# Kernel tuning notes

Hardware: AMD Instinct MI355X
Metric: run time of the kernel (lower is better)

Reference implementation:

```python
import jax, jax.numpy as jnp
import numpy as np

HIDDEN = 4544
NUM_HEADS = 71
HEAD_DIM = 64
SEQ = 2048
ROPE_BASE = 10000.0


def setup_inputs() -> dict:
    key = jax.random.key(0)
    k1, k2, k3 = jax.random.split(key, 3)
    hidden_states = jax.random.normal(k1, (1, 1, SEQ, HIDDEN), dtype=jnp.float32)
    # additive causal mask (0 on/below diagonal, -1e9 above)
    causal = jnp.tril(jnp.ones((SEQ, SEQ), dtype=bool))
    attention_mask = jnp.where(causal, 0.0, -1e9).astype(jnp.float32)[None, None]
    w_qkv = jax.random.normal(k2, (HIDDEN, (NUM_HEADS + 2) * HEAD_DIM), dtype=jnp.float32) * 0.02
    w_dense = jax.random.normal(k3, (HIDDEN, HIDDEN), dtype=jnp.float32) * 0.02
    # RoPE caches as in TtFalconRotaryEmbedding
    inv_freq = 1.0 / (ROPE_BASE ** (jnp.arange(0, HEAD_DIM, 2, dtype=jnp.float32) / HEAD_DIM))
    t = jnp.arange(SEQ, dtype=jnp.float32)
    freqs = jnp.outer(t, inv_freq)                      # [S, HD/2]
    emb = jnp.concatenate([freqs, freqs], axis=-1)      # [S, HD]
    return {
        "hidden_states": hidden_states,
        "attention_mask": attention_mask,
        "w_qkv": w_qkv,
        "w_dense": w_dense,
        "cos": jnp.cos(emb),
        "sin": jnp.sin(emb),
    }


def _rope(x, cos, sin):
    # x: [..., S, HD]; Falcon rotate_half: cat(-x2, x1)
    x1, x2 = jnp.split(x, 2, axis=-1)
    rot = jnp.concatenate([-x2, x1], axis=-1)
    return x * cos + rot * sin


def reference(hidden_states, attention_mask, w_qkv, w_dense, cos, sin):
    S = hidden_states.shape[2]
    x = hidden_states[0, 0]                              # [S, H]
    qkv = (x @ w_qkv).reshape(S, NUM_HEADS + 2, HEAD_DIM)
    q = jnp.transpose(qkv[:, :NUM_HEADS], (1, 0, 2))     # [nh, S, hd]
    k = qkv[:, NUM_HEADS]                                # [S, hd] (single MQA K head)
    v = qkv[:, NUM_HEADS + 1]                            # [S, hd]
    q = _rope(q, cos[None, :S], sin[None, :S])
    k = _rope(k, cos[:S], sin[:S])
    scale = 1.0 / np.sqrt(HEAD_DIM).astype(np.float32)
    scores = jnp.einsum('hsd,td->hst', q, k) * scale + attention_mask[0, 0][None]
    probs = jax.nn.softmax(scores, axis=-1)              # [nh, S, S]
    ctx = jnp.einsum('hst,td->hsd', probs, v)            # [nh, S, hd]
    out = jnp.transpose(ctx, (1, 0, 2)).reshape(S, NUM_HEADS * HEAD_DIM) @ w_dense
    return out[None, None]                               # [1, 1, S, H]
```

## Files before the change

kernel.cpp:

```cpp
#include <hip/hip_runtime.h>

typedef unsigned short u16;
typedef unsigned int u32;
typedef __attribute__((ext_vector_type(8))) __bf16 bf16x8;
typedef __attribute__((ext_vector_type(4))) float f32x4;

#define SEQ   2048
#define NH    71
#define HD    64
#define HID   4544
#define NQKV  4672
#define KP    4608
#define KSL   1536

__device__ __forceinline__ u16 f2bf(float f) {
    __bf16 b = (__bf16)f;
    return __builtin_bit_cast(u16, b);
}
__device__ __forceinline__ float bf2f(u16 u) {
    __bf16 b = __builtin_bit_cast(__bf16, u);
    return (float)b;
}

__device__ __forceinline__ void gload_lds16(const u16* g, u16* l) {
    __builtin_amdgcn_global_load_lds(
        (const __attribute__((address_space(1))) u32*)g,
        (__attribute__((address_space(3))) u32*)l, 16, 0, 0);
}

__global__ __launch_bounds__(256) void k_convert(const float* __restrict__ in,
                                                 u16* __restrict__ out) {
    const int row = blockIdx.x;
    const float* src = in + (size_t)row * HID;
    u16* dst = out + (size_t)row * KP;
    for (int c = threadIdx.x; c < KP / 8; c += 256) {
        u16 o[8];
        if (c < HID / 8) {
            float4 v0 = *(const float4*)(src + c * 8);
            float4 v1 = *(const float4*)(src + c * 8 + 4);
            o[0] = f2bf(v0.x); o[1] = f2bf(v0.y); o[2] = f2bf(v0.z); o[3] = f2bf(v0.w);
            o[4] = f2bf(v1.x); o[5] = f2bf(v1.y); o[6] = f2bf(v1.z); o[7] = f2bf(v1.w);
        } else {
#pragma unroll
            for (int j = 0; j < 8; ++j) o[j] = 0;
        }
        *(uint4*)(dst + c * 8) = *(uint4*)o;
    }
}

__global__ __launch_bounds__(256) void k_transpose(const float* __restrict__ in,
                                                   u16* __restrict__ out,
                                                   int R, int C, int Rp) {
    __shared__ float tile[32][33];
    int c0 = blockIdx.x * 32, r0 = blockIdx.y * 32;
    int tx = threadIdx.x & 31, ty = threadIdx.x >> 5;
#pragma unroll
    for (int i = 0; i < 32; i += 8) {
        int r = r0 + ty + i, c = c0 + tx;
        tile[ty + i][tx] = (r < R && c < C) ? in[(size_t)r * C + c] : 0.f;
    }
    __syncthreads();
#pragma unroll
    for (int i = 0; i < 32; i += 8)
        out[(size_t)(c0 + ty + i) * Rp + r0 + tx] = f2bf(tile[tx][ty + i]);
}

template <bool BF16OUT>
__global__ __launch_bounds__(512) void k_gemm_sk(const u16* __restrict__ A,
                                                 const u16* __restrict__ BT,
                                                 char* __restrict__ C0,
                                                 char* __restrict__ C1,
                                                 char* __restrict__ C2,
                                                 int N, int ntN) {
    __shared__ u16 ls[4][256 * 64];
    const int tid = threadIdx.x;
    const int lane = tid & 63;
    const int wid = tid >> 6;
    const int wr = wid >> 2, wc = wid & 3;
    const int l15 = lane & 15, lg = lane >> 4;

    const int p = blockIdx.x;
    const int m0 = (p & 7) * 256;
    const int rr_ = p >> 3;
    const int ks = rr_ / ntN;
    const int n0 = (rr_ % ntN) * 256;
    const int k0 = ks * KSL;

    const int sg = lane >> 3;
    const int slot = lane & 7;
    const u16* sb[4];
    int dstoff[4];
#pragma unroll
    for (int i = 0; i < 4; ++i) {
        int r = i * 64 + wid * 8 + sg;
        int sc = slot ^ (r & 7);
        sb[i] = (sc < 4) ? (A  + (size_t)(m0 + r) * KP + k0 + sc * 8)
                         : (BT + (size_t)(n0 + r) * KP + k0 + (sc ^ 4) * 8);
        dstoff[i] = r * 64 + slot * 8;
    }

    f32x4 acc[8][4];
#pragma unroll
    for (int i = 0; i < 8; ++i)
#pragma unroll
        for (int j = 0; j < 4; ++j) acc[i][j] = (f32x4){0.f, 0.f, 0.f, 0.f};

#define STG(d, kt, i) gload_lds16(sb[i] + (size_t)(kt) * 32, &ls[d][dstoff[i]])

    const int NT = KSL / 32;
    STG(0, 0, 0); STG(0, 0, 1); STG(0, 0, 2); STG(0, 0, 3);
    STG(1, 1, 0); STG(1, 1, 1); STG(1, 1, 2); STG(1, 1, 3);
    STG(2, 2, 0); STG(2, 2, 1); STG(2, 2, 2); STG(2, 2, 3);
    asm volatile("s_waitcnt vmcnt(8)" ::: "memory");
    __builtin_amdgcn_s_barrier();

    for (int kt = 0; kt < NT; ++kt) {
        const u16* L = ls[kt & 3];
        const int db = (kt + 3) & 3;
        const bool st = (kt + 3 < NT);
        bf16x8 bfr[4], af[4];
#pragma unroll
        for (int ni = 0; ni < 4; ++ni) {
            int rb = wc * 64 + ni * 16 + l15;
            bfr[ni] = *(const bf16x8*)(L + rb * 64 + ((lg ^ (rb & 7) ^ 4) << 3));
        }
#pragma unroll
        for (int mi = 0; mi < 4; ++mi) {
            int ra = wr * 128 + mi * 16 + l15;
            af[mi] = *(const bf16x8*)(L + ra * 64 + ((lg ^ (ra & 7)) << 3));
        }
        if (st) { STG(db, kt + 3, 0); STG(db, kt + 3, 1); }
        __builtin_amdgcn_s_barrier();
        __builtin_amdgcn_s_setprio(1);
#pragma unroll
        for (int mi = 0; mi < 4; ++mi)
#pragma unroll
            for (int ni = 0; ni < 4; ++ni)
                acc[mi][ni] = __builtin_amdgcn_mfma_f32_16x16x32_bf16(
                    af[mi], bfr[ni], acc[mi][ni], 0, 0, 0);
        __builtin_amdgcn_s_setprio(0);
        __builtin_amdgcn_s_barrier();
#pragma unroll
        for (int mi = 0; mi < 4; ++mi) {
            int ra = wr * 128 + (mi + 4) * 16 + l15;
            af[mi] = *(const bf16x8*)(L + ra * 64 + ((lg ^ (ra & 7)) << 3));
        }
        if (st) { STG(db, kt + 3, 2); STG(db, kt + 3, 3); }
        __builtin_amdgcn_s_barrier();
        __builtin_amdgcn_s_setprio(1);
#pragma unroll
        for (int mi = 0; mi < 4; ++mi)
#pragma unroll
            for (int ni = 0; ni < 4; ++ni)
                acc[mi + 4][ni] = __builtin_amdgcn_mfma_f32_16x16x32_bf16(
                    af[mi], bfr[ni], acc[mi + 4][ni], 0, 0, 0);
        __builtin_amdgcn_s_setprio(0);
        if (kt < NT - 3)       asm volatile("s_waitcnt vmcnt(8)" ::: "memory");
        else if (kt == NT - 3) asm volatile("s_waitcnt vmcnt(4)" ::: "memory");
        else if (kt == NT - 2) asm volatile("s_waitcnt vmcnt(0)" ::: "memory");
        __builtin_amdgcn_s_barrier();
    }
#undef STG

    char* Cks = (ks == 0) ? C0 : (ks == 1) ? C1 : C2;
#pragma unroll
    for (int mi = 0; mi < 8; ++mi)
#pragma unroll
        for (int ni = 0; ni < 4; ++ni) {
            int row = m0 + wr * 128 + mi * 16 + lg * 4;
            int col = n0 + wc * 64 + ni * 16 + l15;
            if (col < N) {
                if (BF16OUT) {
                    u16* Cb = (u16*)Cks;
#pragma unroll
                    for (int j = 0; j < 4; ++j)
                        Cb[(size_t)(row + j) * N + col] = f2bf(acc[mi][ni][j]);
                } else {
                    float* Cf = (float*)Cks;
#pragma unroll
                    for (int j = 0; j < 4; ++j)
                        Cf[(size_t)(row + j) * N + col] = acc[mi][ni][j];
                }
            }
        }
}

__global__ __launch_bounds__(256) void k_reduce(float* __restrict__ out,
                                                const float* __restrict__ P1,
                                                const float* __restrict__ P2, int n4) {
    for (int i = blockIdx.x * 256 + threadIdx.x; i < n4; i += gridDim.x * 256) {
        float4 a = ((const float4*)out)[i];
        float4 b = ((const float4*)P1)[i];
        float4 c = ((const float4*)P2)[i];
        a.x += b.x + c.x; a.y += b.y + c.y; a.z += b.z + c.z; a.w += b.w + c.w;
        ((float4*)out)[i] = a;
    }
}

__global__ __launch_bounds__(256) void k_rope(const u16* __restrict__ P0,
                                              const u16* __restrict__ P1,
                                              const u16* __restrict__ P2,
                                              const float* __restrict__ cosb,
                                              const float* __restrict__ sinb,
                                              u16* __restrict__ qb, u16* __restrict__ kb,
                                              u16* __restrict__ vT) {
    int s = blockIdx.x;
    __shared__ float row[NQKV];
    __shared__ float cs[64], sn[64];
    if (threadIdx.x < 64) {
        cs[threadIdx.x] = cosb[s * 64 + threadIdx.x];
        sn[threadIdx.x] = sinb[s * 64 + threadIdx.x];
    }
    const u16* r0 = P0 + (size_t)s * NQKV;
    const u16* r1 = P1 + (size_t)s * NQKV;
    const u16* r2 = P2 + (size_t)s * NQKV;
    for (int e = threadIdx.x; e < NQKV; e += 256)
        row[e] = bf2f(r0[e]) + bf2f(r1[e]) + bf2f(r2[e]);
    __syncthreads();
    const float qscale = 0.125f * 1.44269504f;
    for (int e = threadIdx.x; e < NQKV; e += 256) {
        int h = e >> 6, d = e & 63;
        float x = row[e];
        if (h < 72) {
            float other = row[h * 64 + ((d < 32) ? d + 32 : d - 32)];
            float rot = (d < 32) ? -other : other;
            float rr = x * cs[d] + rot * sn[d];
            if (h < NH) qb[((size_t)h * SEQ + s) * 64 + d] = f2bf(rr * qscale);
            else        kb[(size_t)s * 64 + d] = f2bf(rr);
        } else {
            vT[(size_t)d * SEQ + s] = f2bf(x);
        }
    }
}

__global__ __launch_bounds__(512) void k_attn(const u16* __restrict__ qb,
                                              const u16* __restrict__ kb,
                                              const u16* __restrict__ vT,
                                              u16* __restrict__ ctx) {
    const int tid = threadIdx.x;
    const int lane = tid & 63;
    const int wid = tid >> 6;
    const int l15 = lane & 15, lg = lane >> 4;

    const int bid = blockIdx.x;
    const int qt = 63 - bid / 9;
    const int hg = bid % 9;
    int h = hg * 8 + wid;
    const bool hval = (h < NH);
    if (!hval) h = NH - 1;
    const int q0 = qt * 32;
    const int nt = (qt >> 2) + 1;

    __shared__ u16 lsK[2][128 * 64];
    __shared__ u16 lsV[2][64 * 128];
    __shared__ u16 lsP[8][32 * 128];
    u16* myP = lsP[wid];

    const int kr = tid >> 3, kc = tid & 7;
    const int vd = tid >> 4, vc = tid & 15;

    bf16x8 qf[2][2];
#pragma unroll
    for (int mi = 0; mi < 2; ++mi)
#pragma unroll
        for (int ks = 0; ks < 2; ++ks)
            qf[mi][ks] = *(const bf16x8*)(qb + ((size_t)h * SEQ + q0 + mi * 16 + l15) * 64
                                          + ks * 32 + lg * 8);

    f32x4 oacc[2][4];
#pragma unroll
    for (int i = 0; i < 2; ++i)
#pragma unroll
        for (int j = 0; j < 4; ++j) oacc[i][j] = (f32x4){0.f, 0.f, 0.f, 0.f};
    float mrun[2] = {-3e38f, -3e38f};
    float lrun[2] = {0.f, 0.f};

    uint4 kg0, kg1, vg0, vg1;
    kg0 = *(const uint4*)(kb + (size_t)kr * 64 + kc * 8);
    kg1 = *(const uint4*)(kb + (size_t)(kr + 64) * 64 + kc * 8);
    vg0 = *(const uint4*)(vT + (size_t)vd * SEQ + vc * 8);
    vg1 = *(const uint4*)(vT + (size_t)(vd + 32) * SEQ + vc * 8);
    {
        const int kswz = (kr & 7) << 4;
        *(uint4*)((char*)lsK[0] + kr * 128 + ((kc * 16) ^ kswz)) = kg0;
        *(uint4*)((char*)lsK[0] + (kr + 64) * 128 + ((kc * 16) ^ kswz)) = kg1;
        *(uint4*)((char*)lsV[0] + vd * 256 + ((vc * 16) ^ ((vd & 15) << 4))) = vg0;
        *(uint4*)((char*)lsV[0] + (vd + 32) * 256 + ((vc * 16) ^ (((vd + 32) & 15) << 4))) = vg1;
    }

    for (int t = 0; t < nt; ++t) {
        const int t0 = t << 7;
        const int cb = t & 1;
        if (t + 1 < nt) {
            const int t1 = t0 + 128;
            kg0 = *(const uint4*)(kb + (size_t)(t1 + kr) * 64 + kc * 8);
            kg1 = *(const uint4*)(kb + (size_t)(t1 + kr + 64) * 64 + kc * 8);
            vg0 = *(const uint4*)(vT + (size_t)vd * SEQ + t1 + vc * 8);
            vg1 = *(const uint4*)(vT + (size_t)(vd + 32) * SEQ + t1 + vc * 8);
        }
        __syncthreads();

        f32x4 sacc[2][8];
#pragma unroll
        for (int i = 0; i < 2; ++i)
#pragma unroll
            for (int j = 0; j < 8; ++j) sacc[i][j] = (f32x4){0.f, 0.f, 0.f, 0.f};
#pragma unroll
        for (int ni = 0; ni < 8; ++ni) {
            const int rr = ni * 16 + l15;
            const int swz = (rr & 7) << 4;
            bf16x8 kf0 = *(const bf16x8*)((const char*)lsK[cb] + rr * 128 + ((lg * 16) ^ swz));
            bf16x8 kf1 = *(const bf16x8*)((const char*)lsK[cb] + rr * 128 + ((64 + lg * 16) ^ swz));
            sacc[0][ni] = __builtin_amdgcn_mfma_f32_16x16x32_bf16(kf0, qf[0][0], sacc[0][ni], 0, 0, 0);
            sacc[1][ni] = __builtin_amdgcn_mfma_f32_16x16x32_bf16(kf0, qf[1][0], sacc[1][ni], 0, 0, 0);
            sacc[0][ni] = __builtin_amdgcn_mfma_f32_16x16x32_bf16(kf1, qf[0][1], sacc[0][ni], 0, 0, 0);
            sacc[1][ni] = __builtin_amdgcn_mfma_f32_16x16x32_bf16(kf1, qf[1][1], sacc[1][ni], 0, 0, 0);
        }
        const bool last = (t == nt - 1);

#pragma unroll
        for (int mi = 0; mi < 2; ++mi) {
            const int q = q0 + mi * 16 + l15;
            if (last) {
#pragma unroll
                for (int ni = 0; ni < 8; ++ni)
#pragma unroll
                    for (int jj = 0; jj < 4; ++jj)
                        if (t0 + ni * 16 + lg * 4 + jj > q) sacc[mi][ni][jj] = -1e9f;
            }
            float m = sacc[mi][0][0];
#pragma unroll
            for (int ni = 0; ni < 8; ++ni)
#pragma unroll
                for (int jj = 0; jj < 4; ++jj) m = fmaxf(m, sacc[mi][ni][jj]);
            m = fmaxf(m, __shfl_xor(m, 16, 64));
            m = fmaxf(m, __shfl_xor(m, 32, 64));
            float mnew = fmaxf(mrun[mi], m);
            float alpha = exp2f(mrun[mi] - mnew);
            float rs = 0.f;
#pragma unroll
            for (int ni = 0; ni < 8; ++ni)
#pragma unroll
                for (int jj = 0; jj < 4; ++jj) {
                    float pp = exp2f(sacc[mi][ni][jj] - mnew);
                    sacc[mi][ni][jj] = pp;
                    rs += pp;
                }
            rs += __shfl_xor(rs, 16, 64);
            rs += __shfl_xor(rs, 32, 64);
            lrun[mi] = lrun[mi] * alpha + rs;
            mrun[mi] = mnew;

            const int qh = mi * 16 + l15;
            const int pswz = (qh & 7) << 4;
#pragma unroll
            for (int ni = 0; ni < 8; ++ni) {
                u32 w0 = (u32)f2bf(sacc[mi][ni][0]) | ((u32)f2bf(sacc[mi][ni][1]) << 16);
                u32 w1 = (u32)f2bf(sacc[mi][ni][2]) | ((u32)f2bf(sacc[mi][ni][3]) << 16);
                uint2 w; w.x = w0; w.y = w1;
                *(uint2*)((char*)myP + qh * 256 + ((ni * 32 + lg * 8) ^ pswz)) = w;
            }
#pragma unroll
            for (int jj = 0; jj < 4; ++jj) {
                float aB = __shfl(alpha, (lane & 48) + ((lane >> 4) & 3) * 4 + jj, 64);
#pragma unroll
                for (int nd = 0; nd < 4; ++nd) oacc[mi][nd][jj] *= aB;
            }
        }

#pragma unroll
        for (int ks = 0; ks < 4; ++ks) {
            bf16x8 pf[2];
#pragma unroll
            for (int mi = 0; mi < 2; ++mi) {
                const int qh = mi * 16 + l15;
                pf[mi] = *(const bf16x8*)((const char*)myP + qh * 256
                                          + ((ks * 64 + lg * 16) ^ ((qh & 7) << 4)));
            }
#pragma unroll
            for (int nd = 0; nd < 4; ++nd) {
                const int rr = nd * 16 + l15;
                bf16x8 vf = *(const bf16x8*)((const char*)lsV[cb] + rr * 256
                                             + ((ks * 64 + lg * 16) ^ ((rr & 15) << 4)));
                oacc[0][nd] = __builtin_amdgcn_mfma_f32_16x16x32_bf16(pf[0], vf, oacc[0][nd], 0, 0, 0);
                oacc[1][nd] = __builtin_amdgcn_mfma_f32_16x16x32_bf16(pf[1], vf, oacc[1][nd], 0, 0, 0);
            }
        }

        if (t + 1 < nt) {
            const int nb = cb ^ 1;
            const int kswz = (kr & 7) << 4;
            *(uint4*)((char*)lsK[nb] + kr * 128 + ((kc * 16) ^ kswz)) = kg0;
            *(uint4*)((char*)lsK[nb] + (kr + 64) * 128 + ((kc * 16) ^ kswz)) = kg1;
            *(uint4*)((char*)lsV[nb] + vd * 256 + ((vc * 16) ^ ((vd & 15) << 4))) = vg0;
            *(uint4*)((char*)lsV[nb] + (vd + 32) * 256 + ((vc * 16) ^ (((vd + 32) & 15) << 4))) = vg1;
        }
    }

    if (hval) {
#pragma unroll
        for (int mi = 0; mi < 2; ++mi)
#pragma unroll
            for (int jj = 0; jj < 4; ++jj) {
                float lB = __shfl(lrun[mi], (lane & 48) + ((lane >> 4) & 3) * 4 + jj, 64);
                float inv = 1.0f / lB;
                int q = q0 + mi * 16 + lg * 4 + jj;
#pragma unroll
                for (int nd = 0; nd < 4; ++nd)
                    ctx[(size_t)q * KP + h * 64 + nd * 16 + l15] = f2bf(oacc[mi][nd][jj] * inv);
            }
    } else {
#pragma unroll
        for (int mi = 0; mi < 2; ++mi)
#pragma unroll
            for (int jj = 0; jj < 4; ++jj) {
                int q = q0 + mi * 16 + lg * 4 + jj;
#pragma unroll
                for (int nd = 0; nd < 4; ++nd)
                    ctx[(size_t)q * KP + HID + nd * 16 + l15] = 0;
            }
    }
}

extern "C" void kernel_launch(void* const* d_in, const int* in_sizes, int n_in,
                              void* d_out, int out_size, void* d_ws, size_t ws_size,
                              hipStream_t stream) {
    const float* hs      = (const float*)d_in[0];
    const float* w_qkv   = (const float*)d_in[2];
    const float* w_dense = (const float*)d_in[3];
    const float* cosb    = (const float*)d_in[4];
    const float* sinb    = (const float*)d_in[5];
    float* out = (float*)d_out;

    char* ws = (char*)d_ws;
    u16*   x_bf  = (u16*)(ws + 0);
    u16*   wT    = (u16*)(ws + 18874368);
    char*  qP0   = ws + 63700992;
    char*  qP1   = ws + 82837504;
    char*  qP2   = ws + 101974016;
    u16*   q_bf  = (u16*)(ws + 121110528);
    u16*   k_bf  = (u16*)(ws + 139722752);
    u16*   vT_bf = (u16*)(ws + 139984896);
    char*  dP1   = ws + 63700992;
    char*  dP2   = ws + 100925440;

    k_convert<<<2048, 256, 0, stream>>>(hs, x_bf);
    k_transpose<<<dim3(152, 144), 256, 0, stream>>>(w_qkv, wT, HID, NQKV, KP);
    k_gemm_sk<true><<<dim3(456), 512, 0, stream>>>(x_bf, wT, qP0, qP1, qP2, NQKV, 19);
    k_rope<<<SEQ, 256, 0, stream>>>((const u16*)qP0, (const u16*)qP1, (const u16*)qP2,
                                    cosb, sinb, q_bf, k_bf, vT_bf);
    k_attn<<<dim3(576), 512, 0, stream>>>(q_bf, k_bf, vT_bf, x_bf );
    k_transpose<<<dim3(144, 144), 256, 0, stream>>>(w_dense, wT, HID, HID, KP);
    k_gemm_sk<false><<<dim3(432), 512, 0, stream>>>(x_bf , wT,
                                                    (char*)out, dP1, dP2, HID, 18);
    k_reduce<<<2048, 256, 0, stream>>>(out, (const float*)dP1, (const float*)dP2,
                                       SEQ * HID / 4);
}
```

Measured before the change: 417.1 us.

## Switch split-K GEMM to 32x32x16 MFMA and raise priority in attention MFMA loops

The GEMM inner loop now uses 32x32x16 bf16 MFMA tiles instead of 16x16x32. Each wave covers the same 128x64 output with fewer, larger instructions, and the K=32 step is split into two 16-wide halves with matching LDS fragment loads and a rewritten output indexing. The goal is fewer LDS fragment reads and higher MFMA throughput per instruction. Separately, the attention kernel wraps its QK and PV MFMA blocks in s_setprio so they get scheduling priority over other waves. The risk is higher accumulator register use and mistakes in the new fragment and output mapping.

```diff
diff --git a/kernel.cpp b/kernel.cpp
--- a/kernel.cpp
+++ b/kernel.cpp
@@ -4,6 +4,7 @@
 typedef unsigned int u32;
 typedef __attribute__((ext_vector_type(8))) __bf16 bf16x8;
 typedef __attribute__((ext_vector_type(4))) float f32x4;
+typedef __attribute__((ext_vector_type(16))) float f32x16;
 
 #define SEQ   2048
 #define NH    71
@@ -77,7 +78,7 @@
     const int lane = tid & 63;
     const int wid = tid >> 6;
     const int wr = wid >> 2, wc = wid & 3;
-    const int l15 = lane & 15, lg = lane >> 4;
+    const int l31 = lane & 31, hi = lane >> 5;
 
     const int p = blockIdx.x;
     const int m0 = (p & 7) * 256;
@@ -99,11 +100,11 @@
         dstoff[i] = r * 64 + slot * 8;
     }
 
-    f32x4 acc[8][4];
+    f32x16 acc[8];
 #pragma unroll
     for (int i = 0; i < 8; ++i)
 #pragma unroll
-        for (int j = 0; j < 4; ++j) acc[i][j] = (f32x4){0.f, 0.f, 0.f, 0.f};
+        for (int j = 0; j < 16; ++j) acc[i][j] = 0.f;
 
 #define STG(d, kt, i) gload_lds16(sb[i] + (size_t)(kt) * 32, &ls[d][dstoff[i]])
 
@@ -118,16 +119,16 @@
         const u16* L = ls[kt & 3];
         const int db = (kt + 3) & 3;
         const bool st = (kt + 3 < NT);
-        bf16x8 bfr[4], af[4];
-#pragma unroll
-        for (int ni = 0; ni < 4; ++ni) {
-            int rb = wc * 64 + ni * 16 + l15;
-            bfr[ni] = *(const bf16x8*)(L + rb * 64 + ((lg ^ (rb & 7) ^ 4) << 3));
+        bf16x8 bfr[2], af[4];
+#pragma unroll
+        for (int ni = 0; ni < 2; ++ni) {
+            int rb = wc * 64 + ni * 32 + l31;
+            bfr[ni] = *(const bf16x8*)(L + rb * 64 + (((hi ^ 4) ^ (rb & 7)) << 3));
         }
 #pragma unroll
         for (int mi = 0; mi < 4; ++mi) {
-            int ra = wr * 128 + mi * 16 + l15;
-            af[mi] = *(const bf16x8*)(L + ra * 64 + ((lg ^ (ra & 7)) << 3));
+            int ra = wr * 128 + mi * 32 + l31;
+            af[mi] = *(const bf16x8*)(L + ra * 64 + ((hi ^ (ra & 7)) << 3));
         }
         if (st) { STG(db, kt + 3, 0); STG(db, kt + 3, 1); }
         __builtin_amdgcn_s_barrier();
@@ -135,15 +136,20 @@
 #pragma unroll
         for (int mi = 0; mi < 4; ++mi)
 #pragma unroll
-            for (int ni = 0; ni < 4; ++ni)
-                acc[mi][ni] = __builtin_amdgcn_mfma_f32_16x16x32_bf16(
-                    af[mi], bfr[ni], acc[mi][ni], 0, 0, 0);
+            for (int ni = 0; ni < 2; ++ni)
+                acc[mi * 2 + ni] = __builtin_amdgcn_mfma_f32_32x32x16_bf16(
+                    af[mi], bfr[ni], acc[mi * 2 + ni], 0, 0, 0);
         __builtin_amdgcn_s_setprio(0);
         __builtin_amdgcn_s_barrier();
 #pragma unroll
+        for (int ni = 0; ni < 2; ++ni) {
+            int rb = wc * 64 + ni * 32 + l31;
+            bfr[ni] = *(const bf16x8*)(L + rb * 64 + ((((2 + hi) ^ 4) ^ (rb & 7)) << 3));
+        }
+#pragma unroll
         for (int mi = 0; mi < 4; ++mi) {
-            int ra = wr * 128 + (mi + 4) * 16 + l15;
-            af[mi] = *(const bf16x8*)(L + ra * 64 + ((lg ^ (ra & 7)) << 3));
+            int ra = wr * 128 + mi * 32 + l31;
+            af[mi] = *(const bf16x8*)(L + ra * 64 + (((2 + hi) ^ (ra & 7)) << 3));
         }
         if (st) { STG(db, kt + 3, 2); STG(db, kt + 3, 3); }
         __builtin_amdgcn_s_barrier();
@@ -151,9 +157,9 @@
 #pragma unroll
         for (int mi = 0; mi < 4; ++mi)
 #pragma unroll
-            for (int ni = 0; ni < 4; ++ni)
-                acc[mi + 4][ni] = __builtin_amdgcn_mfma_f32_16x16x32_bf16(
-                    af[mi], bfr[ni], acc[mi + 4][ni], 0, 0, 0);
+            for (int ni = 0; ni < 2; ++ni)
+                acc[mi * 2 + ni] = __builtin_amdgcn_mfma_f32_32x32x16_bf16(
+                    af[mi], bfr[ni], acc[mi * 2 + ni], 0, 0, 0);
         __builtin_amdgcn_s_setprio(0);
         if (kt < NT - 3)       asm volatile("s_waitcnt vmcnt(8)" ::: "memory");
         else if (kt == NT - 3) asm volatile("s_waitcnt vmcnt(4)" ::: "memory");
@@ -164,23 +170,20 @@
 
     char* Cks = (ks == 0) ? C0 : (ks == 1) ? C1 : C2;
 #pragma unroll
-    for (int mi = 0; mi < 8; ++mi)
-#pragma unroll
-        for (int ni = 0; ni < 4; ++ni) {
-            int row = m0 + wr * 128 + mi * 16 + lg * 4;
-            int col = n0 + wc * 64 + ni * 16 + l15;
+    for (int mi = 0; mi < 4; ++mi)
+#pragma unroll
+        for (int ni = 0; ni < 2; ++ni) {
+            int col = n0 + wc * 64 + ni * 32 + l31;
             if (col < N) {
-                if (BF16OUT) {
-                    u16* Cb = (u16*)Cks;
-#pragma unroll
-                    for (int j = 0; j < 4; ++j)
-                        Cb[(size_t)(row + j) * N + col] = f2bf(acc[mi][ni][j]);
-                } else {
-                    float* Cf = (float*)Cks;
-#pragma unroll
-                    for (int j = 0; j < 4; ++j)
-                        Cf[(size_t)(row + j) * N + col] = acc[mi][ni][j];
-                }
+#pragma unroll
+                for (int rg = 0; rg < 4; ++rg)
+#pragma unroll
+                    for (int j = 0; j < 4; ++j) {
+                        int row = m0 + wr * 128 + mi * 32 + rg * 8 + hi * 4 + j;
+                        float v = acc[mi * 2 + ni][rg * 4 + j];
+                        if (BF16OUT) ((u16*)Cks)[(size_t)row * N + col] = f2bf(v);
+                        else         ((float*)Cks)[(size_t)row * N + col] = v;
+                    }
             }
         }
 }
@@ -305,6 +308,7 @@
         for (int i = 0; i < 2; ++i)
 #pragma unroll
             for (int j = 0; j < 8; ++j) sacc[i][j] = (f32x4){0.f, 0.f, 0.f, 0.f};
+        __builtin_amdgcn_s_setprio(1);
 #pragma unroll
         for (int ni = 0; ni < 8; ++ni) {
             const int rr = ni * 16 + l15;
@@ -316,6 +320,7 @@
             sacc[0][ni] = __builtin_amdgcn_mfma_f32_16x16x32_bf16(kf1, qf[0][1], sacc[0][ni], 0, 0, 0);
             sacc[1][ni] = __builtin_amdgcn_mfma_f32_16x16x32_bf16(kf1, qf[1][1], sacc[1][ni], 0, 0, 0);
         }
+        __builtin_amdgcn_s_setprio(0);
         const bool last = (t == nt - 1);
 
 #pragma unroll
@@ -368,6 +373,7 @@
             }
         }
 
+        __builtin_amdgcn_s_setprio(1);
 #pragma unroll
         for (int ks = 0; ks < 4; ++ks) {
             bf16x8 pf[2];
@@ -386,6 +392,7 @@
                 oacc[1][nd] = __builtin_amdgcn_mfma_f32_16x16x32_bf16(pf[1], vf, oacc[1][nd], 0, 0, 0);
             }
         }
+        __builtin_amdgcn_s_setprio(0);
 
         if (t + 1 < nt) {
             const int nb = cb ^ 1;
```

Result: slower. 432.1 us (+3.6%).

## Store dense split-K partials as bf16, add lazy softmax rescale and MFMA priority

Applied to the files above, without the earlier changes.

The dense-projection split-K GEMM now writes all three partial results as bf16 into workspace, and a new reduce kernel sums them into the fp32 output. This replaces the earlier scheme of fp32 partials with a read-modify-write of the output. Less partial traffic is written and read, but each partial is rounded to bf16 before summation, which loses precision. In attention, the running max and the O rescale are only updated when some lane's max rises by more than 8 (in log2 units), saving exp and shuffle work. The MFMA blocks are also wrapped in s_setprio.

```diff
diff --git a/kernel.cpp b/kernel.cpp
--- a/kernel.cpp
+++ b/kernel.cpp
@@ -65,12 +65,11 @@
         out[(size_t)(c0 + ty + i) * Rp + r0 + tx] = f2bf(tile[tx][ty + i]);
 }
 
-template <bool BF16OUT>
 __global__ __launch_bounds__(512) void k_gemm_sk(const u16* __restrict__ A,
                                                  const u16* __restrict__ BT,
-                                                 char* __restrict__ C0,
-                                                 char* __restrict__ C1,
-                                                 char* __restrict__ C2,
+                                                 u16* __restrict__ C0,
+                                                 u16* __restrict__ C1,
+                                                 u16* __restrict__ C2,
                                                  int N, int ntN) {
     __shared__ u16 ls[4][256 * 64];
     const int tid = threadIdx.x;
@@ -162,7 +161,7 @@
     }
 #undef STG
 
-    char* Cks = (ks == 0) ? C0 : (ks == 1) ? C1 : C2;
+    u16* Cks = (ks == 0) ? C0 : (ks == 1) ? C1 : C2;
 #pragma unroll
     for (int mi = 0; mi < 8; ++mi)
 #pragma unroll
@@ -170,30 +169,32 @@
             int row = m0 + wr * 128 + mi * 16 + lg * 4;
             int col = n0 + wc * 64 + ni * 16 + l15;
             if (col < N) {
-                if (BF16OUT) {
-                    u16* Cb = (u16*)Cks;
-#pragma unroll
-                    for (int j = 0; j < 4; ++j)
-                        Cb[(size_t)(row + j) * N + col] = f2bf(acc[mi][ni][j]);
-                } else {
-                    float* Cf = (float*)Cks;
-#pragma unroll
-                    for (int j = 0; j < 4; ++j)
-                        Cf[(size_t)(row + j) * N + col] = acc[mi][ni][j];
-                }
-            }
-        }
-}
-
-__global__ __launch_bounds__(256) void k_reduce(float* __restrict__ out,
-                                                const float* __restrict__ P1,
-                                                const float* __restrict__ P2, int n4) {
-    for (int i = blockIdx.x * 256 + threadIdx.x; i < n4; i += gridDim.x * 256) {
-        float4 a = ((const float4*)out)[i];
-        float4 b = ((const float4*)P1)[i];
-        float4 c = ((const float4*)P2)[i];
-        a.x += b.x + c.x; a.y += b.y + c.y; a.z += b.z + c.z; a.w += b.w + c.w;
-        ((float4*)out)[i] = a;
+#pragma unroll
+                for (int j = 0; j < 4; ++j)
+                    Cks[(size_t)(row + j) * N + col] = f2bf(acc[mi][ni][j]);
+            }
+        }
+}
+
+__global__ __launch_bounds__(256) void k_reduce(const u16* __restrict__ P0,
+                                                const u16* __restrict__ P1,
+                                                const u16* __restrict__ P2,
+                                                float* __restrict__ out, int n8) {
+    for (int i = blockIdx.x * 256 + threadIdx.x; i < n8; i += gridDim.x * 256) {
+        uint4 a = ((const uint4*)P0)[i];
+        uint4 b = ((const uint4*)P1)[i];
+        uint4 c = ((const uint4*)P2)[i];
+        float r[8];
+#pragma unroll
+        for (int j = 0; j < 4; ++j) {
+            u32 aw = (&a.x)[j], bw = (&b.x)[j], cw = (&c.x)[j];
+            r[j * 2]     = bf2f((u16)(aw & 0xffff)) + bf2f((u16)(bw & 0xffff))
+                         + bf2f((u16)(cw & 0xffff));
+            r[j * 2 + 1] = bf2f((u16)(aw >> 16)) + bf2f((u16)(bw >> 16))
+                         + bf2f((u16)(cw >> 16));
+        }
+        ((float4*)out)[i * 2]     = (float4){r[0], r[1], r[2], r[3]};
+        ((float4*)out)[i * 2 + 1] = (float4){r[4], r[5], r[6], r[7]};
     }
 }
 
@@ -305,6 +306,7 @@
         for (int i = 0; i < 2; ++i)
 #pragma unroll
             for (int j = 0; j < 8; ++j) sacc[i][j] = (f32x4){0.f, 0.f, 0.f, 0.f};
+        __builtin_amdgcn_s_setprio(1);
 #pragma unroll
         for (int ni = 0; ni < 8; ++ni) {
             const int rr = ni * 16 + l15;
@@ -316,6 +318,7 @@
             sacc[0][ni] = __builtin_amdgcn_mfma_f32_16x16x32_bf16(kf1, qf[0][1], sacc[0][ni], 0, 0, 0);
             sacc[1][ni] = __builtin_amdgcn_mfma_f32_16x16x32_bf16(kf1, qf[1][1], sacc[1][ni], 0, 0, 0);
         }
+        __builtin_amdgcn_s_setprio(0);
         const bool last = (t == nt - 1);
 
 #pragma unroll
@@ -336,20 +339,32 @@
             m = fmaxf(m, __shfl_xor(m, 16, 64));
             m = fmaxf(m, __shfl_xor(m, 32, 64));
             float mnew = fmaxf(mrun[mi], m);
-            float alpha = exp2f(mrun[mi] - mnew);
+            const bool skiprs = (__all(mnew - mrun[mi] <= 8.0f) != 0);
+            float mref = skiprs ? mrun[mi] : mnew;
             float rs = 0.f;
 #pragma unroll
             for (int ni = 0; ni < 8; ++ni)
 #pragma unroll
                 for (int jj = 0; jj < 4; ++jj) {
-                    float pp = exp2f(sacc[mi][ni][jj] - mnew);
+                    float pp = exp2f(sacc[mi][ni][jj] - mref);
                     sacc[mi][ni][jj] = pp;
                     rs += pp;
                 }
             rs += __shfl_xor(rs, 16, 64);
             rs += __shfl_xor(rs, 32, 64);
-            lrun[mi] = lrun[mi] * alpha + rs;
-            mrun[mi] = mnew;
+            if (skiprs) {
+                lrun[mi] += rs;
+            } else {
+                float alpha = exp2f(mrun[mi] - mnew);
+                lrun[mi] = lrun[mi] * alpha + rs;
+                mrun[mi] = mnew;
+#pragma unroll
+                for (int jj = 0; jj < 4; ++jj) {
+                    float aB = __shfl(alpha, (lane & 48) + ((lane >> 4) & 3) * 4 + jj, 64);
+#pragma unroll
+                    for (int nd = 0; nd < 4; ++nd) oacc[mi][nd][jj] *= aB;
+                }
+            }
 
             const int qh = mi * 16 + l15;
             const int pswz = (qh & 7) << 4;
@@ -360,14 +375,9 @@
                 uint2 w; w.x = w0; w.y = w1;
                 *(uint2*)((char*)myP + qh * 256 + ((ni * 32 + lg * 8) ^ pswz)) = w;
             }
-#pragma unroll
-            for (int jj = 0; jj < 4; ++jj) {
-                float aB = __shfl(alpha, (lane & 48) + ((lane >> 4) & 3) * 4 + jj, 64);
-#pragma unroll
-                for (int nd = 0; nd < 4; ++nd) oacc[mi][nd][jj] *= aB;
-            }
-        }
-
+        }
+
+        __builtin_amdgcn_s_setprio(1);
 #pragma unroll
         for (int ks = 0; ks < 4; ++ks) {
             bf16x8 pf[2];
@@ -386,6 +396,7 @@
                 oacc[1][nd] = __builtin_amdgcn_mfma_f32_16x16x32_bf16(pf[1], vf, oacc[1][nd], 0, 0, 0);
             }
         }
+        __builtin_amdgcn_s_setprio(0);
 
         if (t + 1 < nt) {
             const int nb = cb ^ 1;
@@ -435,24 +446,22 @@
     char* ws = (char*)d_ws;
     u16*   x_bf  = (u16*)(ws + 0);
     u16*   wT    = (u16*)(ws + 18874368);
-    char*  qP0   = ws + 63700992;
-    char*  qP1   = ws + 82837504;
-    char*  qP2   = ws + 101974016;
+    u16*   qP0   = (u16*)(ws + 63700992);
+    u16*   qP1   = (u16*)(ws + 82837504);
+    u16*   qP2   = (u16*)(ws + 101974016);
     u16*   q_bf  = (u16*)(ws + 121110528);
     u16*   k_bf  = (u16*)(ws + 139722752);
     u16*   vT_bf = (u16*)(ws + 139984896);
-    char*  dP1   = ws + 63700992;
-    char*  dP2   = ws + 100925440;
+    u16*   dP0   = (u16*)(ws + 63700992);
+    u16*   dP1   = (u16*)(ws + 82837504);
+    u16*   dP2   = (u16*)(ws + 101974016);
 
     k_convert<<<2048, 256, 0, stream>>>(hs, x_bf);
     k_transpose<<<dim3(152, 144), 256, 0, stream>>>(w_qkv, wT, HID, NQKV, KP);
-    k_gemm_sk<true><<<dim3(456), 512, 0, stream>>>(x_bf, wT, qP0, qP1, qP2, NQKV, 19);
-    k_rope<<<SEQ, 256, 0, stream>>>((const u16*)qP0, (const u16*)qP1, (const u16*)qP2,
-                                    cosb, sinb, q_bf, k_bf, vT_bf);
+    k_gemm_sk<<<dim3(456), 512, 0, stream>>>(x_bf, wT, qP0, qP1, qP2, NQKV, 19);
+    k_rope<<<SEQ, 256, 0, stream>>>(qP0, qP1, qP2, cosb, sinb, q_bf, k_bf, vT_bf);
     k_attn<<<dim3(576), 512, 0, stream>>>(q_bf, k_bf, vT_bf, x_bf );
     k_transpose<<<dim3(144, 144), 256, 0, stream>>>(w_dense, wT, HID, HID, KP);
-    k_gemm_sk<false><<<dim3(432), 512, 0, stream>>>(x_bf , wT,
-                                                    (char*)out, dP1, dP2, HID, 18);
-    k_reduce<<<2048, 256, 0, stream>>>(out, (const float*)dP1, (const float*)dP2,
-                                       SEQ * HID / 4);
-}
+    k_gemm_sk<<<dim3(432), 512, 0, stream>>>(x_bf , wT, dP0, dP1, dP2, HID, 18);
+    k_reduce<<<2048, 256, 0, stream>>>(dP0, dP1, dP2, out, SEQ * HID / 8);
+}
```

New measurement: 406.9 us (median of 3 runs). 1.03x faster.
